# Optimization experiments

Measured on AMD Instinct MI355X. Metric: run time of the kernel, lower is better.

## Reference

```python
import jax, jax.numpy as jnp
import numpy as np

N, E = 20000, 320000          # nodes, edges
R, B = 9, 9                   # num_relations, num_bases
IN, HID, OUT = 128, 256, 64   # feature dims
EPS = 1e-5                    # LayerNorm eps


def layer_norm(h, gamma, beta):
    mu = jnp.mean(h, axis=-1, keepdims=True)
    var = jnp.var(h, axis=-1, keepdims=True)
    return (h - mu) * jax.lax.rsqrt(var + EPS) * gamma + beta


def rgcn_conv(x, src, dst, etype, bases, comp, root, bias, aggr):
    # basis decomposition: W_r = sum_b comp[r,b] * bases[b]
    W = jnp.einsum('rb,bio->rio', comp, bases)          # [R, in, out]
    xW = jnp.einsum('ni,rio->rno', x, W)                # [R, N, out]
    msg = xW[etype, src]                                # [E, out] gather per edge
    if aggr == 'max':
        agg = jax.ops.segment_max(msg, dst, num_segments=N)
        agg = jnp.where(jnp.isfinite(agg), agg, 0.0)    # empty segments -> 0
    else:
        agg = jax.ops.segment_sum(msg, dst, num_segments=N)
    return agg + x @ root + bias


def setup_inputs() -> dict:
    key = jax.random.key(0)
    ks = jax.random.split(key, 12)
    rn = lambda k, s, sc=0.05: jax.random.normal(k, s, jnp.float32) * sc
    return {
        'x': jax.random.normal(ks[0], (N, IN), jnp.float32),
        'edge_index': jax.random.randint(ks[1], (2, E), 0, N),
        'edge_type': jax.random.randint(ks[2], (E,), 0, R),
        # conv1 params
        'bases1': rn(ks[3], (B, IN, HID)),
        'comp1': rn(ks[4], (R, B), 0.3),
        'root1': rn(ks[5], (IN, HID)),
        'bias1': jnp.zeros((HID,), jnp.float32),
        'g1': jnp.ones((HID,), jnp.float32),
        'b1': jnp.zeros((HID,), jnp.float32),
        # conv2 params
        'bases2': rn(ks[6], (B, HID, OUT)),
        'comp2': rn(ks[7], (R, B), 0.3),
        'root2': rn(ks[8], (HID, OUT)),
        'bias2': jnp.zeros((OUT,), jnp.float32),
        'g2': jnp.ones((OUT,), jnp.float32),
        'b2': jnp.zeros((OUT,), jnp.float32),
    }


def reference(x, edge_index, edge_type, bases1, comp1, root1, bias1, g1, b1,
              bases2, comp2, root2, bias2, g2, b2):
    src, dst = edge_index[0], edge_index[1]
    h = rgcn_conv(x, src, dst, edge_type, bases1, comp1, root1, bias1, 'max')
    h = jax.nn.relu(layer_norm(h, g1, b1))
    # eval mode: edge dropout and feature dropout are identity
    h = rgcn_conv(h, src, dst, edge_type, bases2, comp2, root2, bias2, 'add')
    h = layer_norm(h, g2, b2)
    return jax.nn.log_softmax(h, axis=1)
```

## Files before the change

kernel.cpp:

```cpp
#include <hip/hip_runtime.h>
#include <math.h>

#define NN 20000
#define NE 320000
#define NREL 9
#define NBASES 9
#define D_IN 128
#define D_HID 256
#define D_OUT 64
#define LN_EPS 1e-5f

#define N1 (NREL * D_HID + D_HID)
#define N2 (NREL * D_OUT + D_OUT)
#define NBLK ((NN + 255) / 256)

typedef __attribute__((ext_vector_type(8))) short bf16x8;
typedef __attribute__((ext_vector_type(4))) float f32x4;

__device__ inline ushort f2b(float f) {
    unsigned u = __float_as_uint(f);
    return (ushort)((u + 0x7FFFu + ((u >> 16) & 1u)) >> 16);
}
__device__ inline float b2f(ushort h) { return __uint_as_float(((unsigned)h) << 16); }
__device__ inline float b2f_lo(unsigned u) { return __uint_as_float(u << 16); }
__device__ inline float b2f_hi(unsigned u) { return __uint_as_float(u & 0xffff0000u); }
__device__ inline unsigned pack2bf(float f0, float f1) {
    return (unsigned)f2b(f0) | ((unsigned)f2b(f1) << 16);
}

__global__ __launch_bounds__(256) void prep_all(
    const float* __restrict__ bases1, const float* __restrict__ comp1, const float* __restrict__ root1,
    const float* __restrict__ bases2, const float* __restrict__ comp2, const float* __restrict__ root2,
    const float* __restrict__ x, const int* __restrict__ dst,
    ushort* __restrict__ w1t, ushort* __restrict__ w2t, ushort* __restrict__ xbf,
    int* __restrict__ deg)
{
    const int SZW1 = D_IN * D_HID;
    const int SZW2 = D_HID * D_OUT;
    const int SZX  = NN * D_IN;
    int tid = blockIdx.x * 256 + threadIdx.x;
    if (tid < SZW1) {
        int o = tid & (D_HID - 1), k = tid >> 8;
        float acc[NREL];
        #pragma unroll
        for (int r = 0; r < NREL; r++) acc[r] = 0.f;
        #pragma unroll
        for (int b = 0; b < NBASES; b++) {
            float bs = bases1[(b * D_IN + k) * D_HID + o];
            #pragma unroll
            for (int r = 0; r < NREL; r++) acc[r] += comp1[r * NBASES + b] * bs;
        }
        #pragma unroll
        for (int r = 0; r < NREL; r++)
            w1t[(r * D_HID + o) * D_IN + k] = f2b(acc[r]);
        w1t[(NREL * D_HID + o) * D_IN + k] = f2b(root1[k * D_HID + o]);
    } else if (tid < SZW1 + SZW2) {
        int j = tid - SZW1;
        int o = j & (D_OUT - 1), k = j >> 6;
        float acc[NREL];
        #pragma unroll
        for (int r = 0; r < NREL; r++) acc[r] = 0.f;
        #pragma unroll
        for (int b = 0; b < NBASES; b++) {
            float bs = bases2[(b * D_HID + k) * D_OUT + o];
            #pragma unroll
            for (int r = 0; r < NREL; r++) acc[r] += comp2[r * NBASES + b] * bs;
        }
        #pragma unroll
        for (int r = 0; r < NREL; r++)
            w2t[(r * D_OUT + o) * D_HID + k] = f2b(acc[r]);
        w2t[(NREL * D_OUT + o) * D_HID + k] = f2b(root2[k * D_OUT + o]);
    } else if (tid < SZW1 + SZW2 + SZX) {
        int j = tid - SZW1 - SZW2;
        xbf[j] = f2b(x[j]);
    } else if (tid < SZW1 + SZW2 + SZX + NE) {
        int e = tid - SZW1 - SZW2 - SZX;
        atomicAdd(&deg[dst[e]], 1);
    }
}

__global__ __launch_bounds__(256) void scan_blk(
    const int* __restrict__ deg, int* __restrict__ local, int* __restrict__ bsum)
{
    __shared__ int wsum[4];
    int tid = threadIdx.x, lane = tid & 63, w = tid >> 6;
    int i = blockIdx.x * 256 + tid;
    int v = (i < NN) ? deg[i] : 0;
    int x = v;
    #pragma unroll
    for (int d = 1; d < 64; d <<= 1) {
        int y = __shfl_up(x, d, 64);
        if (lane >= d) x += y;
    }
    if (lane == 63) wsum[w] = x;
    __syncthreads();
    int woff = 0;
    for (int j = 0; j < w; j++) woff += wsum[j];
    if (i < NN) local[i] = woff + x - v;
    if (tid == 255) bsum[blockIdx.x] = woff + x;
}

__global__ __launch_bounds__(256) void scan_fin(
    const int* __restrict__ local, const int* __restrict__ bsum,
    int* __restrict__ offs, int* __restrict__ cursor)
{
    __shared__ int boff_s[NBLK];
    int tid = threadIdx.x;
    if (tid < 64) {
        int carry = 0;
        for (int base = 0; base < NBLK; base += 64) {
            int i = base + tid;
            int v = (i < NBLK) ? bsum[i] : 0;
            int x = v;
            #pragma unroll
            for (int d = 1; d < 64; d <<= 1) {
                int y = __shfl_up(x, d, 64);
                if (tid >= d) x += y;
            }
            if (i < NBLK) boff_s[i] = carry + x - v;
            carry += __shfl(x, 63, 64);
        }
    }
    __syncthreads();
    int i = blockIdx.x * 256 + tid;
    if (i < NN) {
        int o = local[i] + boff_s[i >> 8];
        offs[i] = o;
        cursor[i] = o;
    }
    if (i == NN) offs[NN] = NE;
}

__global__ __launch_bounds__(256) void scatter_ep(
    const int* __restrict__ src, const int* __restrict__ dst, const int* __restrict__ etype,
    int* __restrict__ cursor, int* __restrict__ ep1)
{
    int e = blockIdx.x * 256 + threadIdx.x;
    if (e >= NE) return;
    int d = dst[e];
    int s = src[e], r = etype[e];
    int pos = atomicAdd(&cursor[d], 1);
    ep1[pos] = s * N1 + r * D_HID;
}

__global__ __launch_bounds__(512) void gemm_bf16(
    const ushort* __restrict__ A, const ushort* __restrict__ Bt, ushort* __restrict__ C,
    int M, int N, int K)
{
    __shared__ ushort smem[16384];
    ushort* Asb = smem;
    ushort* Bsb = smem + 8192;

    int tid = threadIdx.x;
    int lane = tid & 63, w = tid >> 6;
    int wm = w >> 1, wn = w & 1;
    int row0 = blockIdx.y * 128, col0 = blockIdx.x * 128;

    int r0 = tid >> 2, q0 = tid & 3;
    int mrw = r0 & 15, gw = r0 >> 4;
    int sw = q0 * 16 + ((mrw + 2 * q0) & 15);
    int lo = (gw * 64 + sw) * 8;
    int arow = min(row0 + r0, M - 1);
    const ushort* gA = &A[(size_t)arow * K + q0 * 8];
    const ushort* gB = &Bt[(size_t)(col0 + r0) * K + q0 * 8];

    int mr = lane & 15, kq = lane >> 4;
    int inner = (kq * 16 + ((mr + 2 * kq) & 15)) * 8;

    f32x4 acc[2][4];
    #pragma unroll
    for (int mt = 0; mt < 2; mt++)
        #pragma unroll
        for (int nt = 0; nt < 4; nt++)
            acc[mt][nt] = (f32x4){0.f, 0.f, 0.f, 0.f};

    {
        bf16x8 a0 = *(const bf16x8*)gA;
        bf16x8 b0 = *(const bf16x8*)gB;
        *(bf16x8*)&Asb[lo] = a0;
        *(bf16x8*)&Bsb[lo] = b0;
    }

    const int NC = K >> 5;
    for (int c = 0; c < NC; c++) {
        __syncthreads();
        int cur = c & 1, nxt = cur ^ 1;
        bf16x8 a0, b0;
        bool more = (c + 1 < NC);
        if (more) {
            gA += 32; gB += 32;
            a0 = *(const bf16x8*)gA;
            b0 = *(const bf16x8*)gB;
        }

        bf16x8 af[2], bfr[4];
        #pragma unroll
        for (int mt = 0; mt < 2; mt++)
            af[mt] = *(const bf16x8*)&Asb[cur * 4096 + ((wm * 2 + mt) * 64) * 8 + inner];
        #pragma unroll
        for (int nt = 0; nt < 4; nt++)
            bfr[nt] = *(const bf16x8*)&Bsb[cur * 4096 + ((wn * 4 + nt) * 64) * 8 + inner];
        #pragma unroll
        for (int mt = 0; mt < 2; mt++)
            #pragma unroll
            for (int nt = 0; nt < 4; nt++)
                acc[mt][nt] = __builtin_amdgcn_mfma_f32_16x16x32_bf16(
                    bfr[nt], af[mt], acc[mt][nt], 0, 0, 0);

        if (more) {
            *(bf16x8*)&Asb[nxt * 4096 + lo] = a0;
            *(bf16x8*)&Bsb[nxt * 4096 + lo] = b0;
        }
    }

    __syncthreads();
    int qo = lane >> 4, cm = lane & 15;
    #pragma unroll
    for (int mt = 0; mt < 2; mt++) {
        int row = wm * 32 + mt * 16 + cm;
        int sx = (row & 7) << 3;
        #pragma unroll
        for (int nt = 0; nt < 4; nt++) {
            int colT = wn * 64 + nt * 16 + qo * 4;
            uint2 o;
            o.x = pack2bf(acc[mt][nt][0], acc[mt][nt][1]);
            o.y = pack2bf(acc[mt][nt][2], acc[mt][nt][3]);
            *(uint2*)&smem[(row * 128 + colT) ^ sx] = o;
        }
    }
    __syncthreads();
    #pragma unroll
    for (int i = 0; i < 4; i++) {
        int rr = (tid >> 4) + i * 32;
        int seg = tid & 15;
        uint4 val = *(const uint4*)&smem[(rr * 128 + seg * 8) ^ ((rr & 7) << 3)];
        int gr = row0 + rr;
        if (gr < M)
            *(uint4*)&C[(size_t)gr * N + col0 + seg * 8] = val;
    }
}

__global__ __launch_bounds__(256) void gather1(
    const ushort* __restrict__ xw1, const int* __restrict__ offs, const int* __restrict__ ep1,
    const float* __restrict__ bias, const float* __restrict__ g, const float* __restrict__ b,
    ushort* __restrict__ hout)
{
    int n = blockIdx.x * 4 + (threadIdx.x >> 6);
    if (n >= NN) return;
    int lane = threadIdx.x & 63;
    int hf = lane >> 5;
    int il = lane & 31;
    int cbase = il * 8;
    int e0 = __builtin_amdgcn_readfirstlane(offs[n]);
    int e1 = __builtin_amdgcn_readfirstlane(offs[n + 1]);

    float m[8];
    #pragma unroll
    for (int k = 0; k < 8; k++) m[k] = -INFINITY;

    int e = e0;
    for (; e + 8 <= e1; e += 8) {
        int p[4];
        #pragma unroll
        for (int j = 0; j < 4; j++) p[j] = ep1[e + 2 * j + hf];
        uint4 v[4];
        #pragma unroll
        for (int j = 0; j < 4; j++) v[j] = *(const uint4*)&xw1[(size_t)p[j] + cbase];
        #pragma unroll
        for (int j = 0; j < 4; j++) {
            m[0] = fmaxf(m[0], b2f_lo(v[j].x)); m[1] = fmaxf(m[1], b2f_hi(v[j].x));
            m[2] = fmaxf(m[2], b2f_lo(v[j].y)); m[3] = fmaxf(m[3], b2f_hi(v[j].y));
            m[4] = fmaxf(m[4], b2f_lo(v[j].z)); m[5] = fmaxf(m[5], b2f_hi(v[j].z));
            m[6] = fmaxf(m[6], b2f_lo(v[j].w)); m[7] = fmaxf(m[7], b2f_hi(v[j].w));
        }
    }
    for (; e < e1; e += 2) {
        int ee = min(e + hf, e1 - 1);
        int p = ep1[ee];
        uint4 v = *(const uint4*)&xw1[(size_t)p + cbase];
        m[0] = fmaxf(m[0], b2f_lo(v.x)); m[1] = fmaxf(m[1], b2f_hi(v.x));
        m[2] = fmaxf(m[2], b2f_lo(v.y)); m[3] = fmaxf(m[3], b2f_hi(v.y));
        m[4] = fmaxf(m[4], b2f_lo(v.z)); m[5] = fmaxf(m[5], b2f_hi(v.z));
        m[6] = fmaxf(m[6], b2f_lo(v.w)); m[7] = fmaxf(m[7], b2f_hi(v.w));
    }
    #pragma unroll
    for (int k = 0; k < 8; k++) m[k] = fmaxf(m[k], __shfl_xor(m[k], 32, 64));
    if (e1 == e0) {
        #pragma unroll
        for (int k = 0; k < 8; k++) m[k] = 0.f;
    }

    int c0 = cbase + hf * 4;
    float a0 = hf ? m[4] : m[0];
    float a1 = hf ? m[5] : m[1];
    float a2 = hf ? m[6] : m[2];
    float a3 = hf ? m[7] : m[3];

    ushort4 rt = *(const ushort4*)&xw1[(size_t)n * N1 + NREL * D_HID + c0];
    float t0 = a0 + b2f(rt.x) + bias[c0 + 0];
    float t1 = a1 + b2f(rt.y) + bias[c0 + 1];
    float t2 = a2 + b2f(rt.z) + bias[c0 + 2];
    float t3 = a3 + b2f(rt.w) + bias[c0 + 3];

    float s = t0 + t1 + t2 + t3;
    float s2 = t0 * t0 + t1 * t1 + t2 * t2 + t3 * t3;
    #pragma unroll
    for (int mm = 32; mm >= 1; mm >>= 1) {
        s  += __shfl_xor(s,  mm, 64);
        s2 += __shfl_xor(s2, mm, 64);
    }
    float mu = s * (1.f / D_HID);
    float var = s2 * (1.f / D_HID) - mu * mu;
    float rs = rsqrtf(var + LN_EPS);

    ushort4 o;
    o.x = f2b(fmaxf((t0 - mu) * rs * g[c0 + 0] + b[c0 + 0], 0.f));
    o.y = f2b(fmaxf((t1 - mu) * rs * g[c0 + 1] + b[c0 + 1], 0.f));
    o.z = f2b(fmaxf((t2 - mu) * rs * g[c0 + 2] + b[c0 + 2], 0.f));
    o.w = f2b(fmaxf((t3 - mu) * rs * g[c0 + 3] + b[c0 + 3], 0.f));
    *(ushort4*)&hout[(size_t)n * D_HID + c0] = o;
}

__global__ __launch_bounds__(256) void gather2(
    const ushort* __restrict__ xw2, const int* __restrict__ offs, const int* __restrict__ ep1,
    const float* __restrict__ bias, const float* __restrict__ g, const float* __restrict__ b,
    float* __restrict__ out)
{
    int n = blockIdx.x * 4 + (threadIdx.x >> 6);
    if (n >= NN) return;
    int lane = threadIdx.x & 63;
    int q = lane >> 4;
    int ql = lane & 15;
    int cb = ql * 4;
    int e0 = __builtin_amdgcn_readfirstlane(offs[n]);
    int e1 = __builtin_amdgcn_readfirstlane(offs[n + 1]);

    float s0 = 0.f, s1 = 0.f, s2p = 0.f, s3 = 0.f;
    int e = e0;
    for (; e + 8 <= e1; e += 8) {
        int pa = ep1[e + q] >> 2;
        int pb = ep1[e + 4 + q] >> 2;
        uint2 va = *(const uint2*)&xw2[(size_t)pa + cb];
        uint2 vb = *(const uint2*)&xw2[(size_t)pb + cb];
        s0 += b2f_lo(va.x) + b2f_lo(vb.x);
        s1 += b2f_hi(va.x) + b2f_hi(vb.x);
        s2p += b2f_lo(va.y) + b2f_lo(vb.y);
        s3 += b2f_hi(va.y) + b2f_hi(vb.y);
    }
    for (; e < e1; e += 4) {
        if (e + q < e1) {
            int p = ep1[e + q] >> 2;
            uint2 v = *(const uint2*)&xw2[(size_t)p + cb];
            s0 += b2f_lo(v.x); s1 += b2f_hi(v.x);
            s2p += b2f_lo(v.y); s3 += b2f_hi(v.y);
        }
    }
    s0 += __shfl_xor(s0, 16, 64); s0 += __shfl_xor(s0, 32, 64);
    s1 += __shfl_xor(s1, 16, 64); s1 += __shfl_xor(s1, 32, 64);
    s2p += __shfl_xor(s2p, 16, 64); s2p += __shfl_xor(s2p, 32, 64);
    s3 += __shfl_xor(s3, 16, 64); s3 += __shfl_xor(s3, 32, 64);

    int c = cb + q;
    float agg = (q == 0) ? s0 : (q == 1) ? s1 : (q == 2) ? s2p : s3;
    float v = agg + b2f(xw2[(size_t)n * N2 + NREL * D_OUT + c]) + bias[c];

    float sm = v, sq = v * v;
    #pragma unroll
    for (int mm = 32; mm >= 1; mm >>= 1) {
        sm += __shfl_xor(sm, mm, 64);
        sq += __shfl_xor(sq, mm, 64);
    }
    float mu = sm * (1.f / D_OUT);
    float var = sq * (1.f / D_OUT) - mu * mu;
    float y = (v - mu) * rsqrtf(var + LN_EPS) * g[c] + b[c];

    float mx = y;
    #pragma unroll
    for (int mm = 32; mm >= 1; mm >>= 1) mx = fmaxf(mx, __shfl_xor(mx, mm, 64));
    float ex = __expf(y - mx);
    float se = ex;
    #pragma unroll
    for (int mm = 32; mm >= 1; mm >>= 1) se += __shfl_xor(se, mm, 64);
    out[(size_t)n * D_OUT + c] = y - mx - logf(se);
}

extern "C" void kernel_launch(void* const* d_in, const int* in_sizes, int n_in,
                              void* d_out, int out_size, void* d_ws, size_t ws_size,
                              hipStream_t stream)
{
    const float* x      = (const float*)d_in[0];
    const int*   eidx   = (const int*)  d_in[1];
    const int*   etype  = (const int*)  d_in[2];
    const float* bases1 = (const float*)d_in[3];
    const float* comp1  = (const float*)d_in[4];
    const float* root1  = (const float*)d_in[5];
    const float* bias1  = (const float*)d_in[6];
    const float* g1     = (const float*)d_in[7];
    const float* b1     = (const float*)d_in[8];
    const float* bases2 = (const float*)d_in[9];
    const float* comp2  = (const float*)d_in[10];
    const float* root2  = (const float*)d_in[11];
    const float* bias2  = (const float*)d_in[12];
    const float* g2     = (const float*)d_in[13];
    const float* b2     = (const float*)d_in[14];

    const int* src = eidx;
    const int* dst = eidx + NE;

    char* p = (char*)d_ws;
    auto alloc = [&](size_t bytes) -> char* {
        char* r = p;
        p += (bytes + 255) & ~(size_t)255;
        return r;
    };
    ushort* xbf    = (ushort*)alloc((size_t)NN * D_IN * 2);
    ushort* w1t    = (ushort*)alloc((size_t)N1 * D_IN * 2);
    ushort* w2t    = (ushort*)alloc((size_t)N2 * D_HID * 2);
    ushort* xw1    = (ushort*)alloc((size_t)NN * N1 * 2);
    ushort* xw2    = (ushort*)alloc((size_t)NN * N2 * 2);
    ushort* h      = (ushort*)alloc((size_t)NN * D_HID * 2);
    int*    deg    = (int*)   alloc((size_t)NN * 4);
    int*    local  = (int*)   alloc((size_t)NN * 4);
    int*    bsum   = (int*)   alloc((size_t)NBLK * 4);
    int*    offs   = (int*)   alloc((size_t)(NN + 1) * 4);
    int*    cursor = (int*)   alloc((size_t)NN * 4);
    int*    ep1    = (int*)   alloc((size_t)NE * 4);

    hipMemsetAsync(deg, 0, (size_t)NN * 4, stream);
    const int SZP = D_IN * D_HID + D_HID * D_OUT + NN * D_IN + NE;
    prep_all<<<(SZP + 255) / 256, 256, 0, stream>>>(
        bases1, comp1, root1, bases2, comp2, root2, x, dst, w1t, w2t, xbf, deg);

    scan_blk<<<NBLK, 256, 0, stream>>>(deg, local, bsum);
    scan_fin<<<NBLK, 256, 0, stream>>>(local, bsum, offs, cursor);
    scatter_ep<<<(NE + 255) / 256, 256, 0, stream>>>(src, dst, etype, cursor, ep1);

    gemm_bf16<<<dim3(N1 / 128, (NN + 127) / 128), 512, 0, stream>>>(xbf, w1t, xw1, NN, N1, D_IN);
    gather1<<<(NN + 3) / 4, 256, 0, stream>>>(xw1, offs, ep1, bias1, g1, b1, h);

    gemm_bf16<<<dim3(N2 / 128, (NN + 127) / 128), 512, 0, stream>>>(h, w2t, xw2, NN, N2, D_HID);
    gather2<<<(NN + 3) / 4, 256, 0, stream>>>(xw2, offs, ep1, bias2, g2, b2, (float*)d_out);
}
```

Baseline: 219.7 us.

## Vectorize x conversion, remap GEMM blocks per XCD, use nontemporal output stores

```diff
diff --git a/kernel.cpp b/kernel.cpp
--- a/kernel.cpp
+++ b/kernel.cpp
@@ -16,6 +16,7 @@
 
 typedef __attribute__((ext_vector_type(8))) short bf16x8;
 typedef __attribute__((ext_vector_type(4))) float f32x4;
+typedef __attribute__((ext_vector_type(4))) unsigned int u32x4;
 
 __device__ inline ushort f2b(float f) {
     unsigned u = __float_as_uint(f);
@@ -37,7 +38,7 @@
 {
     const int SZW1 = D_IN * D_HID;
     const int SZW2 = D_HID * D_OUT;
-    const int SZX  = NN * D_IN;
+    const int SZX4 = NN * D_IN / 4;
     int tid = blockIdx.x * 256 + threadIdx.x;
     if (tid < SZW1) {
         int o = tid & (D_HID - 1), k = tid >> 8;
@@ -70,11 +71,14 @@
         for (int r = 0; r < NREL; r++)
             w2t[(r * D_OUT + o) * D_HID + k] = f2b(acc[r]);
         w2t[(NREL * D_OUT + o) * D_HID + k] = f2b(root2[k * D_OUT + o]);
-    } else if (tid < SZW1 + SZW2 + SZX) {
+    } else if (tid < SZW1 + SZW2 + SZX4) {
         int j = tid - SZW1 - SZW2;
-        xbf[j] = f2b(x[j]);
-    } else if (tid < SZW1 + SZW2 + SZX + NE) {
-        int e = tid - SZW1 - SZW2 - SZX;
+        float4 v = *(const float4*)&x[(size_t)j * 4];
+        ushort4 o;
+        o.x = f2b(v.x); o.y = f2b(v.y); o.z = f2b(v.z); o.w = f2b(v.w);
+        *(ushort4*)&xbf[(size_t)j * 4] = o;
+    } else if (tid < SZW1 + SZW2 + SZX4 + NE) {
+        int e = tid - SZW1 - SZW2 - SZX4;
         atomicAdd(&deg[dst[e]], 1);
     }
 }
@@ -151,10 +155,17 @@
     ushort* Asb = smem;
     ushort* Bsb = smem + 8192;
 
+    int nwg = gridDim.x * gridDim.y;
+    int o = blockIdx.y * gridDim.x + blockIdx.x;
+    int q = nwg >> 3, r = nwg & 7;
+    int xcd = o & 7, idx = o >> 3;
+    int wk = (xcd < r ? xcd * (q + 1) : r * (q + 1) + (xcd - r) * q) + idx;
+    int bx = wk % gridDim.x, by = wk / gridDim.x;
+
     int tid = threadIdx.x;
     int lane = tid & 63, w = tid >> 6;
     int wm = w >> 1, wn = w & 1;
-    int row0 = blockIdx.y * 128, col0 = blockIdx.x * 128;
+    int row0 = by * 128, col0 = bx * 128;
 
     int r0 = tid >> 2, q0 = tid & 3;
     int mrw = r0 & 15, gw = r0 >> 4;
@@ -222,10 +233,10 @@
         #pragma unroll
         for (int nt = 0; nt < 4; nt++) {
             int colT = wn * 64 + nt * 16 + qo * 4;
-            uint2 o;
-            o.x = pack2bf(acc[mt][nt][0], acc[mt][nt][1]);
-            o.y = pack2bf(acc[mt][nt][2], acc[mt][nt][3]);
-            *(uint2*)&smem[(row * 128 + colT) ^ sx] = o;
+            uint2 oo;
+            oo.x = pack2bf(acc[mt][nt][0], acc[mt][nt][1]);
+            oo.y = pack2bf(acc[mt][nt][2], acc[mt][nt][3]);
+            *(uint2*)&smem[(row * 128 + colT) ^ sx] = oo;
         }
     }
     __syncthreads();
@@ -233,10 +244,10 @@
     for (int i = 0; i < 4; i++) {
         int rr = (tid >> 4) + i * 32;
         int seg = tid & 15;
-        uint4 val = *(const uint4*)&smem[(rr * 128 + seg * 8) ^ ((rr & 7) << 3)];
+        u32x4 val = *(const u32x4*)&smem[(rr * 128 + seg * 8) ^ ((rr & 7) << 3)];
         int gr = row0 + rr;
         if (gr < M)
-            *(uint4*)&C[(size_t)gr * N + col0 + seg * 8] = val;
+            __builtin_nontemporal_store(val, (u32x4*)&C[(size_t)gr * N + col0 + seg * 8]);
     }
 }
 
@@ -427,7 +438,7 @@
     int*    ep1    = (int*)   alloc((size_t)NE * 4);
 
     hipMemsetAsync(deg, 0, (size_t)NN * 4, stream);
-    const int SZP = D_IN * D_HID + D_HID * D_OUT + NN * D_IN + NE;
+    const int SZP = D_IN * D_HID + D_HID * D_OUT + NN * D_IN / 4 + NE;
     prep_all<<<(SZP + 255) / 256, 256, 0, stream>>>(
         bases1, comp1, root1, bases2, comp2, root2, x, dst, w1t, w2t, xbf, deg);
 
```

New measurement: 222.5 us. Within noise of the previous version (+1.3%).
